# Kernel optimization log

Hardware: AMD Instinct MI355X
Metric: run time of the kernel (lower is better)

Reference implementation:

```python
import jax, jax.numpy as jnp
import numpy as np

N, T, D, H = 16, 1024, 1024, 1024


def setup_inputs() -> dict:
    key = jax.random.key(0)
    ks = jax.random.split(key, 7)
    x = jax.random.normal(ks[0], (N, T, D), dtype=jnp.float32)
    reset = jax.random.randint(ks[1], (N, T), 0, 2).astype(bool)
    carry = jax.random.normal(ks[2], (N, T, H), dtype=jnp.float32)
    # learned parameters (orthogonal-ish init approximated by scaled gaussian)
    initial_h = jax.random.normal(ks[3], (H,), dtype=jnp.float32) * 0.1
    w_i = jax.random.normal(ks[4], (D, 3 * H), dtype=jnp.float32) * (1.0 / np.sqrt(D))
    w_h = jax.random.normal(ks[5], (H, 3 * H), dtype=jnp.float32) * (1.0 / np.sqrt(H))
    b = jnp.zeros((3 * H,), dtype=jnp.float32)
    return {"x": x, "reset": reset, "carry": carry,
            "initial_h": initial_h, "w_i": w_i, "w_h": w_h, "b": b}


def _gru_scan(x, reset, carry, initial_h, w_i, w_h, b):
    n, t, _ = x.shape
    h_dim = initial_h.shape[0]
    # learn_initial_h and not is_target: replace carry with learned init where reset
    init_b = jnp.broadcast_to(initial_h, (n, t, h_dim))
    carry = jnp.where(reset[..., None], init_b, carry)
    # precompute input projections for all timesteps (math-equivalent hoist)
    gx = jnp.einsum('ntd,dk->ntk', x, w_i)  # [N,T,3H]
    w_h_zr, w_h_a = w_h[:, :2 * h_dim], w_h[:, 2 * h_dim:]
    b_zr, b_a = b[:2 * h_dim], b[2 * h_dim:]

    def step(h, inp):
        gx_t, reset_t, carry_t = inp  # [N,3H], [N], [N,H]
        h = jnp.where(reset_t[:, None], carry_t, h)
        zr = jax.nn.sigmoid(gx_t[:, :2 * h_dim] + h @ w_h_zr + b_zr)
        z, r = zr[:, :h_dim], zr[:, h_dim:]
        a = jnp.tanh(gx_t[:, 2 * h_dim:] + (r * h) @ w_h_a + b_a)
        h_next = (1.0 - z) * h + z * a
        return h_next, h_next

    h0 = carry[:, 0, :]  # scan init is carry_seq[:1,:] per batch element
    _, hs = jax.lax.scan(step, h0, (gx.transpose(1, 0, 2), reset.T, carry.transpose(1, 0, 2)))
    states = hs.transpose(1, 0, 2)  # [N,T,H]
    return states


def reference(x, reset, carry, initial_h, w_i, w_h, b):
    states = _gru_scan(x, reset, carry, initial_h, w_i, w_h, b)
    # hk.GRU returns (next_state, next_state): outputs_seq == states_seq
    return states, states, initial_h[None, :]
```

## Files before the change

### kernel.cpp

```cpp
#include <hip/hip_runtime.h>

typedef __attribute__((ext_vector_type(8))) short s8v;
typedef __attribute__((ext_vector_type(4))) float f4v;
typedef __attribute__((ext_vector_type(4))) unsigned int u4v;
typedef unsigned long long u64;

__device__ __forceinline__ float bf2f(unsigned short u) {
    union { float f; unsigned int i; } v; v.i = ((unsigned int)u) << 16; return v.f;
}
__device__ __forceinline__ unsigned short f2bf(float f) {
    union { float f; unsigned int i; } v; v.f = f;
    unsigned int x = v.i;
    return (unsigned short)((x + 0x7fffu + ((x >> 16) & 1u)) >> 16);
}
__device__ __forceinline__ float ldf(const void* p, size_t i, int f32) {
    return f32 ? ((const float*)p)[i] : bf2f(((const unsigned short*)p)[i]);
}

__device__ __forceinline__ s8v ald16(u64* p) {
    union { s8v v; u64 u[2]; } r;
    r.u[0] = __hip_atomic_load(p,     __ATOMIC_RELAXED, __HIP_MEMORY_SCOPE_AGENT);
    r.u[1] = __hip_atomic_load(p + 1, __ATOMIC_RELAXED, __HIP_MEMORY_SCOPE_AGENT);
    return r.v;
}
__device__ __forceinline__ void pack_store64(u64* p, int lane, unsigned short val) {
    unsigned int mv = val;
    unsigned int lo = mv | (__shfl_down(mv, 16, 64) << 16);
    unsigned int hi = __shfl_down(mv, 32, 64) | (__shfl_down(mv, 48, 64) << 16);
    if (lane < 16) {
        u64 q = (u64)lo | ((u64)hi << 32);
        __hip_atomic_store(p, q, __ATOMIC_RELAXED, __HIP_MEMORY_SCOPE_AGENT);
    }
}

__device__ __forceinline__ void pollwait(int* f, int v) {
    while (__hip_atomic_load(f, __ATOMIC_RELAXED, __HIP_MEMORY_SCOPE_AGENT) < v)
        __builtin_amdgcn_s_sleep(1);
    __builtin_amdgcn_sched_barrier(0);
    asm volatile("" ::: "memory");
}

__global__ void detect_k(const unsigned short* __restrict__ xu,
                         const unsigned int* __restrict__ rw,
                         int* __restrict__ flags) {
    __shared__ int cnt;
    int tid = threadIdx.x;
    if (tid == 0) cnt = 0;
    for (int i = tid + 16; i < 528; i += 256) flags[i] = 0;
    __syncthreads();
    int bad = 0;
    for (int i = tid; i < 4096; i += 256) {
        unsigned short v = xu[i];
        int e = (v >> 7) & 0xFF;
        if (e == 0xFF || (e <= 90 && (v & 0x7FFFu) != 0)) bad++;
    }
    atomicAdd(&cnt, bad);
    __syncthreads();
    if (tid == 0) {
        flags[0] = (cnt > 16) ? 1 : 0;
        bool w01 = true, oddz = true, ones = false, b01 = true, h16 = true, fv = true;
        for (int i = 0; i < 32; ++i) {
            unsigned int w = rw[i];
            if (w > 1u) w01 = false;
            if ((i & 1) && w != 0u) oddz = false;
            if (w != 0u) ones = true;
            if ((w & 0xFFu) > 1u || ((w >> 8) & 0xFFu) > 1u ||
                ((w >> 16) & 0xFFu) > 1u || (w >> 24) > 1u) b01 = false;
            unsigned int lo = w & 0xFFFFu, hi = w >> 16;
            if (!((lo == 0u || lo == 0x3F80u) && (hi == 0u || hi == 0x3F80u))) h16 = false;
            if (!(w == 0u || w == 0x3F800000u)) fv = false;
        }
        int mode;
        if (w01 && oddz && ones) mode = 4;
        else if (w01) mode = 0;
        else if (fv) mode = 3;
        else if (h16) mode = 2;
        else if (b01) mode = 1;
        else mode = 0;
        flags[1] = mode;
    }
}

__device__ __forceinline__ int get_reset(const void* p, int mode, int idx) {
    switch (mode) {
        case 0: return ((const int*)p)[idx] != 0;
        case 1: return ((const signed char*)p)[idx] != 0;
        case 2: return ((const unsigned short*)p)[idx] != 0;
        case 3: return ((const float*)p)[idx] != 0.f;
        default: return ((const int*)p)[idx * 2] != 0;
    }
}

__device__ __forceinline__ void stage_w(const void* w, int wf32, int j0, int tid,
                                        unsigned short* lws) {
    for (int k = tid; k < 1024; k += 256) {
        #pragma unroll
        for (int g = 0; g < 3; ++g) {
            unsigned short tmp[8];
            size_t base = (size_t)k * 3072 + g * 1024 + j0;
            if (wf32) {
                const float* wf = (const float*)w;
                f4v v0 = *(const f4v*)&wf[base];
                f4v v1 = *(const f4v*)&wf[base + 4];
                #pragma unroll
                for (int r = 0; r < 4; ++r) { tmp[r] = f2bf(v0[r]); tmp[4 + r] = f2bf(v1[r]); }
            } else {
                union { u4v v; unsigned short u[8]; } cv;
                cv.v = *(const u4v*)&((const unsigned short*)w)[base];
                #pragma unroll
                for (int r = 0; r < 8; ++r) tmp[r] = cv.u[r];
            }
            #pragma unroll
            for (int r = 0; r < 8; ++r) lws[(g * 8 + r) * 1048 + k] = tmp[r];
        }
    }
}

__global__ __launch_bounds__(256) void scan_k(
    const void* __restrict__ xv, const void* __restrict__ resetv,
    const void* __restrict__ carryv, const void* __restrict__ inithv,
    const void* __restrict__ wiv, const void* __restrict__ whv,
    const void* __restrict__ biasv, void* __restrict__ outv,
    unsigned short* __restrict__ hbuf0, unsigned short* __restrict__ hbuf1,
    unsigned short* __restrict__ rbuf0, unsigned short* __restrict__ rbuf1,
    int* __restrict__ flags) {
    __shared__ __align__(16) unsigned short lws[24 * 1048];
    __shared__ __align__(16) float lpartA[4 * 256];
    __shared__ __align__(16) float lpartB[4 * 256];
    __shared__ float lhe[128];

    const int xf32 = flags[0];
    const int rmode = flags[1];
    int* flagA = flags + 16;
    int* flagB = flags + 272;

    const int tid = threadIdx.x;
    const int wave = tid >> 6, lane = tid & 63;
    const int c = lane & 15, q = lane >> 4;
    const int j0 = blockIdx.x * 8;
    const int an = tid & 15, ac = tid >> 4;
    const int jloc = ac & 7, jg = j0 + jloc;
    const bool owner = (ac < 8);
    const int colA = owner ? jg : (1024 + jg);
    const int colB = 2048 + jg;
    const float biasA = ldf(biasv, colA, xf32);
    const float biasB = ldf(biasv, colB, xf32);
    const float initj = ldf(inithv, jg, xf32);
    const unsigned short initj_b = f2bf(initj);
    const int kbase = wave * 256;
    const int qidx = an * 256 + (j0 >> 2) + (wave & 1);

    s8v whA[8], whB[8], wiA[8], wiB[8];
    stage_w(whv, xf32, j0, tid, lws);
    __syncthreads();
    #pragma unroll
    for (int kc = 0; kc < 8; ++kc) {
        int kk = kbase + kc * 32 + q * 8;
        whA[kc] = *(const s8v*)&lws[c * 1048 + kk];
        whB[kc] = *(const s8v*)&lws[(16 + (c & 7)) * 1048 + kk];
    }
    __syncthreads();
    stage_w(wiv, xf32, j0, tid, lws);
    __syncthreads();
    #pragma unroll
    for (int kc = 0; kc < 8; ++kc) {
        int kk = kbase + kc * 32 + q * 8;
        wiA[kc] = *(const s8v*)&lws[c * 1048 + kk];
        wiB[kc] = *(const s8v*)&lws[(16 + (c & 7)) * 1048 + kk];
    }

    s8v xa[8];
    auto load_xa = [&](int tt) {
        if (xf32) {
            const float* xf = (const float*)xv;
            #pragma unroll
            for (int kc = 0; kc < 8; ++kc) {
                size_t b = (size_t)c * 1048576 + (size_t)tt * 1024 + kbase + kc * 32 + q * 8;
                f4v v0 = *(const f4v*)&xf[b];
                f4v v1 = *(const f4v*)&xf[b + 4];
                union { s8v v; unsigned short u[8]; } cv;
                #pragma unroll
                for (int r = 0; r < 4; ++r) { cv.u[r] = f2bf(v0[r]); cv.u[4 + r] = f2bf(v1[r]); }
                xa[kc] = cv.v;
            }
        } else {
            const unsigned short* xu = (const unsigned short*)xv;
            #pragma unroll
            for (int kc = 0; kc < 8; ++kc) {
                size_t b = (size_t)c * 1048576 + (size_t)tt * 1024 + kbase + kc * 32 + q * 8;
                xa[kc] = *(const s8v*)&xu[b];
            }
        }
    };

    float hreg = 0.f, zreg = 0.f, he_own = 0.f;
    int rs_cur = 0;
    if (owner) {
        rs_cur = get_reset(resetv, rmode, an * 1024);
        float h0 = rs_cur ? initj : ldf(carryv, (size_t)an * 1048576 + jg, xf32);
        unsigned short hb0 = f2bf(h0);
        hreg = bf2f(hb0);
        pack_store64((u64*)hbuf0 + qidx, lane, hb0);
        if (an == 0) {
            if (xf32) ((float*)outv)[(size_t)33554432 + jg] = initj;
            else ((unsigned short*)outv)[(size_t)33554432 + jg] = initj_b;
        }
        asm volatile("s_waitcnt vmcnt(0)" ::: "memory");
        if (lane == 0)
            __hip_atomic_store(&flagB[blockIdx.x * 2 + wave], 1,
                               __ATOMIC_RELAXED, __HIP_MEMORY_SCOPE_AGENT);
    }
    load_xa(0);

    for (int t = 0; t < 1024; ++t) {
        unsigned short* hcur = (t & 1) ? hbuf1 : hbuf0;
        unsigned short* hnxt = (t & 1) ? hbuf0 : hbuf1;
        unsigned short* rcur = (t & 1) ? rbuf1 : rbuf0;

        int rs_next = 0;
        if (owner) {
            he_own = rs_cur ? initj : hreg;
            lhe[an * 8 + jloc] = he_own;
            if (t < 1023) rs_next = get_reset(resetv, rmode, an * 1024 + t + 1);
        }

        f4v acc = (f4v){0.f, 0.f, 0.f, 0.f};
        #pragma unroll
        for (int kc = 0; kc < 8; ++kc)
            acc = __builtin_amdgcn_mfma_f32_16x16x32_bf16(xa[kc], wiA[kc], acc, 0, 0, 0);

        pollwait(&flagB[tid], t + 1);
        s8v ha[8];
        #pragma unroll
        for (int kc = 0; kc < 8; ++kc)
            ha[kc] = ald16((u64*)hcur + ((c * 1024 + kbase + kc * 32 + q * 8) >> 2));
        #pragma unroll
        for (int kc = 0; kc < 8; ++kc)
            acc = __builtin_amdgcn_mfma_f32_16x16x32_bf16(ha[kc], whA[kc], acc, 0, 0, 0);
        *(f4v*)&lpartA[wave * 256 + c * 16 + q * 4] = acc;
        __syncthreads();
        {
            float pre = lpartA[ac * 16 + an] + lpartA[256 + ac * 16 + an] +
                        lpartA[512 + ac * 16 + an] + lpartA[768 + ac * 16 + an] + biasA;
            float sg = 1.f / (1.f + expf(-pre));
            if (owner) zreg = sg;
            else {
                pack_store64((u64*)rcur + qidx, lane, f2bf(sg * lhe[an * 8 + jloc]));
                asm volatile("s_waitcnt vmcnt(0)" ::: "memory");
                if (lane == 0)
                    __hip_atomic_store(&flagA[blockIdx.x * 2 + (wave - 2)], t + 1,
                                       __ATOMIC_RELAXED, __HIP_MEMORY_SCOPE_AGENT);
            }
        }

        f4v acc2 = (f4v){0.f, 0.f, 0.f, 0.f};
        #pragma unroll
        for (int kc = 0; kc < 8; ++kc)
            acc2 = __builtin_amdgcn_mfma_f32_16x16x32_bf16(xa[kc], wiB[kc], acc2, 0, 0, 0);

        pollwait(&flagA[tid], t + 1);
        s8v ra[8];
        #pragma unroll
        for (int kc = 0; kc < 8; ++kc)
            ra[kc] = ald16((u64*)rcur + ((c * 1024 + kbase + kc * 32 + q * 8) >> 2));
        #pragma unroll
        for (int kc = 0; kc < 8; ++kc)
            acc2 = __builtin_amdgcn_mfma_f32_16x16x32_bf16(ra[kc], whB[kc], acc2, 0, 0, 0);
        *(f4v*)&lpartB[wave * 256 + c * 16 + q * 4] = acc2;
        __syncthreads();
        if (owner) {
            float preB = lpartB[ac * 16 + an] + lpartB[256 + ac * 16 + an] +
                         lpartB[512 + ac * 16 + an] + lpartB[768 + ac * 16 + an] + biasB;
            float aa = tanhf(preB);
            float hn = (1.f - zreg) * he_own + zreg * aa;
            unsigned short hb = f2bf(hn);
            hreg = hn;
            pack_store64((u64*)hnxt + qidx, lane, rs_next ? initj_b : hb);
            asm volatile("s_waitcnt vmcnt(0)" ::: "memory");
            if (lane == 0)
                __hip_atomic_store(&flagB[blockIdx.x * 2 + wave], t + 2,
                                   __ATOMIC_RELAXED, __HIP_MEMORY_SCOPE_AGENT);
            size_t oidx = ((size_t)an * 1024 + t) * 1024 + jg;
            if (xf32) {
                float* o = (float*)outv;
                o[oidx] = hn;
                o[16777216 + oidx] = hn;
            } else {
                unsigned short* o = (unsigned short*)outv;
                o[oidx] = hb;
                o[16777216 + oidx] = hb;
            }
            rs_cur = rs_next;
        }
        if (t < 1023) load_xa(t + 1);
    }
}

extern "C" void kernel_launch(void* const* d_in, const int* in_sizes, int n_in,
                              void* d_out, int out_size, void* d_ws, size_t ws_size,
                              hipStream_t stream) {
    const void* x     = d_in[0];
    const void* reset = d_in[1];
    const void* carry = d_in[2];
    const void* inith = d_in[3];
    const void* w_i   = d_in[4];
    const void* w_h   = d_in[5];
    const void* bias  = d_in[6];

    char* ws = (char*)d_ws;
    unsigned short* hbuf0 = (unsigned short*)ws;
    unsigned short* hbuf1 = (unsigned short*)(ws + 32768);
    unsigned short* rbuf0 = (unsigned short*)(ws + 65536);
    unsigned short* rbuf1 = (unsigned short*)(ws + 98304);
    int*            flags = (int*)(ws + 131072);

    detect_k<<<dim3(1), dim3(256), 0, stream>>>(
        (const unsigned short*)x, (const unsigned int*)reset, flags);

    void* kargs[] = { (void*)&x, (void*)&reset, (void*)&carry, (void*)&inith,
                      (void*)&w_i, (void*)&w_h, (void*)&bias, (void*)&d_out,
                      (void*)&hbuf0, (void*)&hbuf1, (void*)&rbuf0, (void*)&rbuf1,
                      (void*)&flags };
    hipError_t err = hipLaunchCooperativeKernel(
        reinterpret_cast<const void*>(&scan_k),
        dim3(128), dim3(256), kargs, 0, stream);
    (void)err; (void)in_sizes; (void)n_in; (void)out_size; (void)ws_size;
}
```

Before: 14.46 ms.

## Run GRU scan on 64 blocks with fused input projection and fallback kernel

Adds a new cooperative scan kernel that uses 64 blocks, each owning 16 hidden columns. Each block keeps both the recurrent and input weight slices in registers and computes the x@W_i projection with MFMA inside the time loop. Halving the block count is meant to cut inter-block flag synchronisation overhead per step, and overlapping the input projection with the waits for other blocks hides latency. The original 128-block kernel stays as a fallback that exits early when the new kernel sets a completion flag. This adds an extra launch and more register pressure per block.

```diff
diff --git a/kernel.cpp b/kernel.cpp
--- a/kernel.cpp
+++ b/kernel.cpp
@@ -46,7 +46,7 @@
     __shared__ int cnt;
     int tid = threadIdx.x;
     if (tid == 0) cnt = 0;
-    for (int i = tid + 16; i < 528; i += 256) flags[i] = 0;
+    for (int i = tid + 8; i < 528; i += 256) flags[i] = 0;
     __syncthreads();
     int bad = 0;
     for (int i = tid; i < 4096; i += 256) {
@@ -116,7 +116,7 @@
     }
 }
 
-__global__ __launch_bounds__(256) void scan_k(
+__global__ __launch_bounds__(256, 1) void scan64_k(
     const void* __restrict__ xv, const void* __restrict__ resetv,
     const void* __restrict__ carryv, const void* __restrict__ inithv,
     const void* __restrict__ wiv, const void* __restrict__ whv,
@@ -124,6 +124,208 @@
     unsigned short* __restrict__ hbuf0, unsigned short* __restrict__ hbuf1,
     unsigned short* __restrict__ rbuf0, unsigned short* __restrict__ rbuf1,
     int* __restrict__ flags) {
+    __shared__ __align__(16) unsigned short lws[24 * 1048];
+    __shared__ __align__(16) float lpA[2 * 1024];
+    __shared__ __align__(16) float lpB[1024];
+
+    const int xf32 = flags[0];
+    const int rmode = flags[1];
+    int* flagA = flags + 16;
+    int* flagB = flags + 272;
+
+    const int tid = threadIdx.x;
+    const int wave = tid >> 6, lane = tid & 63;
+    const int c = lane & 15, q = lane >> 4;
+    const int j0 = blockIdx.x * 16;
+    const int an = tid & 15, jloc = tid >> 4;
+    const int jg = j0 + jloc;
+    const float biasZ = ldf(biasv, jg, xf32);
+    const float biasR = ldf(biasv, 1024 + jg, xf32);
+    const float biasA = ldf(biasv, 2048 + jg, xf32);
+    const float initj = ldf(inithv, jg, xf32);
+    const unsigned short initj_b = f2bf(initj);
+    const int kbase = wave * 256;
+    const int qidx = an * 256 + (j0 >> 2) + wave;
+
+    s8v whZ[8], whR[8], whA[8], wiZ[8], wiR[8], wiA[8];
+    #pragma unroll
+    for (int p = 0; p < 2; ++p) {
+        stage_w(whv, xf32, j0 + 8 * p, tid, lws);
+        __syncthreads();
+        if ((c >> 3) == p) {
+            int cz = c & 7;
+            #pragma unroll
+            for (int kc = 0; kc < 8; ++kc) {
+                int kk = kbase + kc * 32 + q * 8;
+                whZ[kc] = *(const s8v*)&lws[cz * 1048 + kk];
+                whR[kc] = *(const s8v*)&lws[(8 + cz) * 1048 + kk];
+                whA[kc] = *(const s8v*)&lws[(16 + cz) * 1048 + kk];
+            }
+        }
+        __syncthreads();
+    }
+    #pragma unroll
+    for (int p = 0; p < 2; ++p) {
+        stage_w(wiv, xf32, j0 + 8 * p, tid, lws);
+        __syncthreads();
+        if ((c >> 3) == p) {
+            int cz = c & 7;
+            #pragma unroll
+            for (int kc = 0; kc < 8; ++kc) {
+                int kk = kbase + kc * 32 + q * 8;
+                wiZ[kc] = *(const s8v*)&lws[cz * 1048 + kk];
+                wiR[kc] = *(const s8v*)&lws[(8 + cz) * 1048 + kk];
+                wiA[kc] = *(const s8v*)&lws[(16 + cz) * 1048 + kk];
+            }
+        }
+        __syncthreads();
+    }
+
+    s8v xa[8];
+    auto load_xa = [&](int tt) {
+        if (xf32) {
+            const float* xf = (const float*)xv;
+            #pragma unroll
+            for (int kc = 0; kc < 8; ++kc) {
+                size_t b = (size_t)c * 1048576 + (size_t)tt * 1024 + kbase + kc * 32 + q * 8;
+                f4v v0 = *(const f4v*)&xf[b];
+                f4v v1 = *(const f4v*)&xf[b + 4];
+                union { s8v v; unsigned short u[8]; } cv;
+                #pragma unroll
+                for (int r = 0; r < 4; ++r) { cv.u[r] = f2bf(v0[r]); cv.u[4 + r] = f2bf(v1[r]); }
+                xa[kc] = cv.v;
+            }
+        } else {
+            const unsigned short* xu = (const unsigned short*)xv;
+            #pragma unroll
+            for (int kc = 0; kc < 8; ++kc) {
+                size_t b = (size_t)c * 1048576 + (size_t)tt * 1024 + kbase + kc * 32 + q * 8;
+                xa[kc] = *(const s8v*)&xu[b];
+            }
+        }
+    };
+
+    float hreg, zreg = 0.f, he_own = 0.f;
+    int rs_cur = get_reset(resetv, rmode, an * 1024);
+    {
+        float h0 = rs_cur ? initj : ldf(carryv, (size_t)an * 1048576 + jg, xf32);
+        unsigned short hb0 = f2bf(h0);
+        hreg = bf2f(hb0);
+        pack_store64((u64*)hbuf0 + qidx, lane, hb0);
+        if (an == 0) {
+            if (xf32) ((float*)outv)[(size_t)33554432 + jg] = initj;
+            else ((unsigned short*)outv)[(size_t)33554432 + jg] = initj_b;
+        }
+        asm volatile("s_waitcnt vmcnt(0)" ::: "memory");
+        if (lane == 0)
+            __hip_atomic_store(&flagB[blockIdx.x * 4 + wave], 1,
+                               __ATOMIC_RELAXED, __HIP_MEMORY_SCOPE_AGENT);
+    }
+    load_xa(0);
+
+    for (int t = 0; t < 1024; ++t) {
+        unsigned short* hcur = (t & 1) ? hbuf1 : hbuf0;
+        unsigned short* hnxt = (t & 1) ? hbuf0 : hbuf1;
+        unsigned short* rcur = (t & 1) ? rbuf1 : rbuf0;
+
+        he_own = rs_cur ? initj : hreg;
+        int rs_next = (t < 1023) ? get_reset(resetv, rmode, an * 1024 + t + 1) : 0;
+
+        f4v accZ = (f4v){0.f, 0.f, 0.f, 0.f};
+        f4v accR = (f4v){0.f, 0.f, 0.f, 0.f};
+        #pragma unroll
+        for (int kc = 0; kc < 8; ++kc) {
+            accZ = __builtin_amdgcn_mfma_f32_16x16x32_bf16(xa[kc], wiZ[kc], accZ, 0, 0, 0);
+            accR = __builtin_amdgcn_mfma_f32_16x16x32_bf16(xa[kc], wiR[kc], accR, 0, 0, 0);
+        }
+        pollwait(&flagB[tid], t + 1);
+        s8v ha[8];
+        #pragma unroll
+        for (int kc = 0; kc < 8; ++kc)
+            ha[kc] = ald16((u64*)hcur + ((c * 1024 + kbase + kc * 32 + q * 8) >> 2));
+        #pragma unroll
+        for (int kc = 0; kc < 8; ++kc) {
+            accZ = __builtin_amdgcn_mfma_f32_16x16x32_bf16(ha[kc], whZ[kc], accZ, 0, 0, 0);
+            accR = __builtin_amdgcn_mfma_f32_16x16x32_bf16(ha[kc], whR[kc], accR, 0, 0, 0);
+        }
+        *(f4v*)&lpA[wave * 256 + c * 16 + q * 4] = accZ;
+        *(f4v*)&lpA[1024 + wave * 256 + c * 16 + q * 4] = accR;
+        __syncthreads();
+        {
+            float zpre = lpA[jloc * 16 + an] + lpA[256 + jloc * 16 + an] +
+                         lpA[512 + jloc * 16 + an] + lpA[768 + jloc * 16 + an] + biasZ;
+            float rpre = lpA[1024 + jloc * 16 + an] + lpA[1280 + jloc * 16 + an] +
+                         lpA[1536 + jloc * 16 + an] + lpA[1792 + jloc * 16 + an] + biasR;
+            zreg = 1.f / (1.f + expf(-zpre));
+            float rg = 1.f / (1.f + expf(-rpre));
+            pack_store64((u64*)rcur + qidx, lane, f2bf(rg * he_own));
+            asm volatile("s_waitcnt vmcnt(0)" ::: "memory");
+            if (lane == 0)
+                __hip_atomic_store(&flagA[blockIdx.x * 4 + wave], t + 1,
+                                   __ATOMIC_RELAXED, __HIP_MEMORY_SCOPE_AGENT);
+        }
+
+        f4v acc2 = (f4v){0.f, 0.f, 0.f, 0.f};
+        #pragma unroll
+        for (int kc = 0; kc < 8; ++kc)
+            acc2 = __builtin_amdgcn_mfma_f32_16x16x32_bf16(xa[kc], wiA[kc], acc2, 0, 0, 0);
+        pollwait(&flagA[tid], t + 1);
+        s8v ra[8];
+        #pragma unroll
+        for (int kc = 0; kc < 8; ++kc)
+            ra[kc] = ald16((u64*)rcur + ((c * 1024 + kbase + kc * 32 + q * 8) >> 2));
+        #pragma unroll
+        for (int kc = 0; kc < 8; ++kc)
+            acc2 = __builtin_amdgcn_mfma_f32_16x16x32_bf16(ra[kc], whA[kc], acc2, 0, 0, 0);
+        *(f4v*)&lpB[wave * 256 + c * 16 + q * 4] = acc2;
+        __syncthreads();
+        {
+            float preB = lpB[jloc * 16 + an] + lpB[256 + jloc * 16 + an] +
+                         lpB[512 + jloc * 16 + an] + lpB[768 + jloc * 16 + an] + biasA;
+            float aa = tanhf(preB);
+            float hn = (1.f - zreg) * he_own + zreg * aa;
+            unsigned short hb = f2bf(hn);
+            hreg = hn;
+            pack_store64((u64*)hnxt + qidx, lane, rs_next ? initj_b : hb);
+            asm volatile("s_waitcnt vmcnt(0)" ::: "memory");
+            if (lane == 0)
+                __hip_atomic_store(&flagB[blockIdx.x * 4 + wave], t + 2,
+                                   __ATOMIC_RELAXED, __HIP_MEMORY_SCOPE_AGENT);
+            size_t oidx = ((size_t)an * 1024 + t) * 1024 + jg;
+            if (xf32) {
+                float* o = (float*)outv;
+                o[oidx] = hn;
+                o[16777216 + oidx] = hn;
+            } else {
+                unsigned short* o = (unsigned short*)outv;
+                o[oidx] = hb;
+                o[16777216 + oidx] = hb;
+            }
+            rs_cur = rs_next;
+        }
+        if (t < 1023) load_xa(t + 1);
+    }
+
+    if (blockIdx.x == 0) {
+        pollwait(&flagB[tid], 1025);
+        __syncthreads();
+        if (tid == 0)
+            __hip_atomic_store(&flags[8], 1,
+                               __ATOMIC_RELAXED, __HIP_MEMORY_SCOPE_AGENT);
+    }
+}
+
+__global__ __launch_bounds__(256) void scan_fb(
+    const void* __restrict__ xv, const void* __restrict__ resetv,
+    const void* __restrict__ carryv, const void* __restrict__ inithv,
+    const void* __restrict__ wiv, const void* __restrict__ whv,
+    const void* __restrict__ biasv, void* __restrict__ outv,
+    unsigned short* __restrict__ hbuf0, unsigned short* __restrict__ hbuf1,
+    unsigned short* __restrict__ rbuf0, unsigned short* __restrict__ rbuf1,
+    int* __restrict__ flags) {
+    if (__hip_atomic_load(&flags[8], __ATOMIC_RELAXED,
+                          __HIP_MEMORY_SCOPE_AGENT) != 0) return;
+
     __shared__ __align__(16) unsigned short lws[24 * 1048];
     __shared__ __align__(16) float lpartA[4 * 256];
     __shared__ __align__(16) float lpartB[4 * 256];
@@ -321,8 +523,16 @@
                       (void*)&w_i, (void*)&w_h, (void*)&bias, (void*)&d_out,
                       (void*)&hbuf0, (void*)&hbuf1, (void*)&rbuf0, (void*)&rbuf1,
                       (void*)&flags };
-    hipError_t err = hipLaunchCooperativeKernel(
-        reinterpret_cast<const void*>(&scan_k),
+
+    hipError_t e64 = hipLaunchCooperativeKernel(
+        reinterpret_cast<const void*>(&scan64_k),
+        dim3(64), dim3(256), kargs, 0, stream);
+    (void)e64;
+
+    hipError_t efb = hipLaunchCooperativeKernel(
+        reinterpret_cast<const void*>(&scan_fb),
         dim3(128), dim3(256), kargs, 0, stream);
-    (void)err; (void)in_sizes; (void)n_in; (void)out_size; (void)ws_size;
-}
+    (void)efb;
+
+    (void)in_sizes; (void)n_in; (void)out_size; (void)ws_size;
+}
```

Measured after the change: 15.39 ms. 6.4% more time.
